# Performance work log

Measured on AMD Instinct MI355X. Metric: run time of the kernel, lower is better.

## Reference

```python
import jax, jax.numpy as jnp
import numpy as np

B, TX, TY = 32, 64, 64
E = H = 1024
VEN = VCN = 32000


def _lstm_scan(x_gates, Whh, bhh, h0, c0):
    # x_gates: [T, B, 4H] precomputed input contribution (x @ Wih.T + bih)
    def step(carry, xg_t):
        h, c = carry
        gates = xg_t + h @ Whh.T + bhh  # [B, 4H]
        i, f, g, o = jnp.split(gates, 4, axis=-1)  # torch gate order i,f,g,o
        c = jax.nn.sigmoid(f) * c + jax.nn.sigmoid(i) * jnp.tanh(g)
        h = jax.nn.sigmoid(o) * jnp.tanh(c)
        return (h, c), (h, c)
    (hT, cT), (hs, cs) = jax.lax.scan(step, (h0, c0), x_gates)
    return hs, cs, hT, cT  # hs/cs: [T, B, H]


def setup_inputs() -> dict:
    key = jax.random.key(0)
    ks = jax.random.split(key, 12)
    u = lambda k, shp, s: jax.random.uniform(k, shp, jnp.float32, -s, s)
    s = 1.0 / np.sqrt(H)
    return {
        "x": jax.random.randint(ks[0], (B, TX), 0, VEN, dtype=jnp.int32),
        "x_mask": jnp.ones((B, TX), dtype=jnp.int32),
        "y": jax.random.randint(ks[1], (B, TY), 0, VCN, dtype=jnp.int32),
        "h0": jnp.zeros((B, H), jnp.float32),
        "c0": jnp.zeros((B, H), jnp.float32),
        "emb_en": u(ks[2], (VEN, E), 0.1),
        "emb_cn": u(ks[3], (VCN, E), 0.1),
        "Wih_e": u(ks[4], (4 * H, E), s),
        "Whh_e": u(ks[5], (4 * H, H), s),
        "bih_e": jnp.zeros((4 * H,), jnp.float32),
        "bhh_e": jnp.zeros((4 * H,), jnp.float32),
        "Wih_d": u(ks[6], (4 * H, E), s),
        "Whh_d": u(ks[7], (4 * H, H), s),
        "bih_d": jnp.zeros((4 * H,), jnp.float32),
        "bhh_d": jnp.zeros((4 * H,), jnp.float32),
        "Wout": u(ks[8], (VCN, H), 0.1),
        "bout": jnp.zeros((VCN,), jnp.float32),
    }


def reference(x, x_mask, y, h0, c0, emb_en, emb_cn,
              Wih_e, Whh_e, bih_e, bhh_e,
              Wih_d, Whh_d, bih_d, bhh_d, Wout, bout):
    # --- encoder: per-timestep LSTMCell unrolled via lax.scan ---
    xe = emb_en[x]  # [B, Tx, E]
    xg = jnp.einsum('bte,ge->tbg', xe, Wih_e) + bih_e  # [Tx, B, 4H]
    hs, cs, _, _ = _lstm_scan(xg, Whh_e, bhh_e, h0, c0)  # [Tx, B, H]
    # pick hidden/cell at last valid timestep (mask.sum - 1)
    lengths = jnp.sum(x_mask, axis=1) - 1  # [B]
    bidx = jnp.arange(x.shape[0])
    h = hs[lengths, bidx]  # [B, H]
    c = cs[lengths, bidx]
    # --- decoder: single-layer LSTM ---
    ye = emb_cn[y]  # [B, Ty, E]
    yg = jnp.einsum('bte,ge->tbg', ye, Wih_d) + bih_d  # [Ty, B, 4H]
    dh, _, _, _ = _lstm_scan(yg, Whh_d, bhh_d, h, c)  # [Ty, B, H]
    hiddens = jnp.transpose(dh, (1, 0, 2))  # [B, Ty, H]
    logits = jnp.einsum('bth,vh->btv', hiddens, Wout) + bout  # [B, Ty, V]
    decoded = jax.nn.log_softmax(logits, axis=-1)
    return decoded, hiddens
```

## Files before the change

kernel.cpp:

```cpp
#include <hip/hip_runtime.h>

typedef __attribute__((ext_vector_type(8))) short bf16x8;
typedef __attribute__((ext_vector_type(4))) float fx4;
typedef __attribute__((ext_vector_type(4))) unsigned short u16x4;
typedef __attribute__((ext_vector_type(8))) unsigned short u16x8;
typedef __attribute__((ext_vector_type(4))) unsigned int u32x4;

#define DEV static __device__ __forceinline__

DEV unsigned short f2bf(float f) {
  union { float f; unsigned u; } v; v.f = f;
  unsigned u = v.u;
  u += 0x7fffu + ((u >> 16) & 1u);
  return (unsigned short)(u >> 16);
}
DEV unsigned pk(float a, float b) { return (unsigned)f2bf(a) | ((unsigned)f2bf(b) << 16); }
DEV float sigm(float x) { return 1.f / (1.f + __expf(-x)); }

DEV u32x4 load_coh16(const void* p) {
  u32x4 r;
  asm volatile("global_load_dwordx4 %0, %1, off sc0 sc1" : "=v"(r) : "v"(p));
  return r;
}

typedef __attribute__((address_space(1))) const unsigned int guint;
typedef __attribute__((address_space(3))) unsigned int luint;
DEV void gload_lds16(const void* g, void* l) {
  __builtin_amdgcn_global_load_lds((guint*)g, (luint*)l, 16, 0, 0);
}

__global__ void k_gather2(const float* __restrict__ embE, const int* __restrict__ tokE,
                          unsigned short* __restrict__ dstE,
                          const float* __restrict__ embC, const int* __restrict__ tokC,
                          unsigned short* __restrict__ dstC) {
  int bid = blockIdx.x;
  int r = bid & 2047;
  const float* emb = bid < 2048 ? embE : embC;
  const int* tok = bid < 2048 ? tokE : tokC;
  unsigned short* dst = bid < 2048 ? dstE : dstC;
  int t = r >> 5, b = r & 31;
  int token = tok[b * 64 + t];
  const fx4* srow = (const fx4*)(emb + (long)token * 1024);
  u16x4* drow = (u16x4*)(dst + (long)r * 1024);
  fx4 v = srow[threadIdx.x];
  u16x4 o = { f2bf(v[0]), f2bf(v[1]), f2bf(v[2]), f2bf(v[3]) };
  drow[threadIdx.x] = o;
}

__global__ void k_lengths(const int* __restrict__ mask, int* __restrict__ sel,
                          int* __restrict__ bar) {
  int t = threadIdx.x;
  for (int i = t; i < 4096; i += 256) bar[i] = 0;
  if (t < 32) {
    int s = 0;
    for (int k = 0; k < 64; ++k) s += mask[t * 64 + k];
    sel[t] = (s + 63) & 63;
  }
}

__global__ void k_f2bf_dual(const float* __restrict__ s0, unsigned short* __restrict__ d0,
                            const float* __restrict__ s1, unsigned short* __restrict__ d1,
                            long n4) {
  const float* s = blockIdx.x < 1024 ? s0 : s1;
  unsigned short* d = blockIdx.x < 1024 ? d0 : d1;
  long base = (long)(blockIdx.x & 1023) * 256 + threadIdx.x;
  for (long i = base; i < n4; i += 1024 * 256) {
    fx4 v = ((const fx4*)s)[i];
    u16x4 o = { f2bf(v[0]), f2bf(v[1]), f2bf(v[2]), f2bf(v[3]) };
    ((u16x4*)d)[i] = o;
  }
}

#define SCAN_NBLK 64

template<int MODE>
__global__ __launch_bounds__(512) void k_scan(
    const float* __restrict__ Whh,
    const float* __restrict__ bhh,
    const float* __restrict__ xg,
    const float* __restrict__ hinit,
    const float* __restrict__ cinit,
    unsigned short* __restrict__ hbuf,
    const int* __restrict__ sel,
    float* __restrict__ hsel, float* __restrict__ csel,
    float* __restrict__ hid_out,
    unsigned short* __restrict__ hid_bf,
    int* __restrict__ bar,
    const float* __restrict__ wsrc,
    unsigned short* __restrict__ wdst,
    long wn4) {
  int tid = threadIdx.x;
  int bid = blockIdx.x;
  if (bid >= SCAN_NBLK) {
    long i = (long)(bid - SCAN_NBLK) * 512 + tid;
    long st = (long)(gridDim.x - SCAN_NBLK) * 512;
    for (; i < wn4; i += st) {
      fx4 v = ((const fx4*)wsrc)[i];
      u16x4 o = { f2bf(v[0]), f2bf(v[1]), f2bf(v[2]), f2bf(v[3]) };
      ((u16x4*)wdst)[i] = o;
    }
    return;
  }
  __shared__ __align__(16) unsigned short hlds[49152];
  __shared__ float gbuf[4][32][16];
  int j0 = ((bid & 7) * 8 + (bid >> 3)) * 16;
  int w = tid >> 6, lane = tid & 63;
  int mt = w & 1, nt = w >> 1;
  int fr = lane & 15, fg = lane >> 4;
  unsigned* hbU = (unsigned*)hbuf;
  constexpr int GBASE = MODE ? 64 : 0;

  bf16x8 breg[32];
  {
    const float* wrow = Whh + ((long)(nt * 1024 + j0 + fr) << 10);
#pragma unroll
    for (int i = 0; i < 32; ++i) {
      int kc = i * 4 + fg;
      fx4 lo = *(const fx4*)(wrow + kc * 8);
      fx4 hi = *(const fx4*)(wrow + kc * 8 + 4);
      bf16x8 o = { (short)f2bf(lo[0]), (short)f2bf(lo[1]), (short)f2bf(lo[2]), (short)f2bf(lo[3]),
                   (short)f2bf(hi[0]), (short)f2bf(hi[1]), (short)f2bf(hi[2]), (short)f2bf(hi[3]) };
      breg[i] = o;
    }
  }

  int b = tid >> 4, jj = tid & 15, j = j0 + jj;
  float bh0 = bhh[j], bh1 = bhh[1024 + j], bh2 = bhh[2048 + j], bh3 = bhh[3072 + j];
  float c_reg = cinit[b * 1024 + j];
  int sel_b = (MODE == 0) ? sel[b] : -1;
  const float* xp0 = xg + (long)b * 4096 + j;
  float x0 = xp0[0], x1 = xp0[1024], x2 = xp0[2048], x3 = xp0[3072];

  for (int t = 0; t < 64; ++t) {
    if (t == 0) {
#pragma unroll
      for (int it = 0; it < 8; ++it) {
        int c = it * 512 + tid;
        const float* src = hinit + (long)c * 8;
        fx4 lo = *(const fx4*)src;
        fx4 hi = *(const fx4*)(src + 4);
        int row = c >> 7, kc = c & 127;
        u16x8 o = { f2bf(lo[0]), f2bf(lo[1]), f2bf(lo[2]), f2bf(lo[3]),
                    f2bf(hi[0]), f2bf(hi[1]), f2bf(hi[2]), f2bf(hi[3]) };
        *(u16x8*)&hlds[(row * 128 + (kc ^ (row & 31))) * 8] = o;
      }
    } else {
      const char* hsrc = (const char*)hbuf + (t & 1) * 65536;
      u32x4 hv[8];
#pragma unroll
      for (int it = 0; it < 8; ++it) {
        int c = it * 512 + tid;
        hv[it] = load_coh16(hsrc + (long)c * 16);
      }
      asm volatile("s_waitcnt vmcnt(0)" ::: "memory");
      __builtin_amdgcn_sched_barrier(0);
#pragma unroll
      for (int it = 0; it < 8; ++it) {
        int c = it * 512 + tid;
        int row = c >> 7, kc = c & 127;
        *(u16x8*)&hlds[(row * 128 + (kc ^ (row & 31))) * 8] = *(u16x8*)&hv[it];
      }
    }
    __syncthreads();

    int arow = mt * 16 + fr;
    fx4 acca = {0.f, 0.f, 0.f, 0.f}, accb = {0.f, 0.f, 0.f, 0.f};
#pragma unroll
    for (int i = 0; i < 32; i += 2) {
      int kcA = i * 4 + fg;
      int kcB = (i + 1) * 4 + fg;
      bf16x8 a0 = *(const bf16x8*)&hlds[(arow * 128 + (kcA ^ (arow & 31))) * 8];
      bf16x8 a1 = *(const bf16x8*)&hlds[(arow * 128 + (kcB ^ (arow & 31))) * 8];
      acca = __builtin_amdgcn_mfma_f32_16x16x32_bf16(a0, breg[i], acca, 0, 0, 0);
      accb = __builtin_amdgcn_mfma_f32_16x16x32_bf16(a1, breg[i + 1], accb, 0, 0, 0);
    }
#pragma unroll
    for (int q = 0; q < 4; ++q)
      gbuf[nt][mt * 16 + fg * 4 + q][fr] = acca[q] + accb[q];
    __syncthreads();

    {
      float gi = gbuf[0][b][jj] + bh0 + x0;
      float gf = gbuf[1][b][jj] + bh1 + x1;
      float gg = gbuf[2][b][jj] + bh2 + x2;
      float go = gbuf[3][b][jj] + bh3 + x3;
      float c_new = sigm(gf) * c_reg + sigm(gi) * tanhf(gg);
      float h = sigm(go) * tanhf(c_new);
      c_reg = c_new;
      float hp = __shfl_xor(h, 1);
      if ((jj & 1) == 0) {
        unsigned val = pk(h, hp);
        __hip_atomic_store(&hbU[((t & 1) ^ 1) * 16384 + b * 512 + ((j0 + jj) >> 1)], val,
                           __ATOMIC_RELAXED, __HIP_MEMORY_SCOPE_AGENT);
      }
      if (MODE == 0) {
        if (t == sel_b) { hsel[b * 1024 + j] = h; csel[b * 1024 + j] = c_new; }
      } else {
        long o = ((long)b * 64 + t) * 1024 + j;
        hid_out[o] = h;
        if (hid_bf) hid_bf[o] = f2bf(h);
      }
    }

    if (t < 63) {
      const float* xp = xg + (long)(t + 1) * 131072 + (long)b * 4096 + j;
      float nx0 = xp[0], nx1 = xp[1024], nx2 = xp[2048], nx3 = xp[3072];
      __syncthreads();
      if (w == 0) {
        if (lane == 0)
          __hip_atomic_store(&bar[bid * 32], GBASE + t + 1, __ATOMIC_RELAXED, __HIP_MEMORY_SCOPE_AGENT);
        int want = GBASE + t + 1;
        for (;;) {
          int v0 = __hip_atomic_load(&bar[lane * 32], __ATOMIC_RELAXED, __HIP_MEMORY_SCOPE_AGENT);
          if (__ballot(v0 >= want) == 0xFFFFFFFFFFFFFFFFULL) break;
          __builtin_amdgcn_s_sleep(1);
        }
      }
      __syncthreads();
      x0 = nx0; x1 = nx1; x2 = nx2; x3 = nx3;
    }
  }
}

__global__ __launch_bounds__(256) void k_gemm_dual(
    const unsigned short* __restrict__ A0, const unsigned short* __restrict__ B0,
    const float* __restrict__ bias0, float* __restrict__ C0,
    const unsigned short* __restrict__ A1, const unsigned short* __restrict__ B1,
    const float* __restrict__ bias1, float* __restrict__ C1) {
  __shared__ __align__(16) unsigned short As[2][4096];
  __shared__ __align__(16) unsigned short Bs[2][4096];
  int lid = blockIdx.x;
  int half = lid >> 9, l = lid & 511;
  const unsigned short* A = half ? A1 : A0;
  const unsigned short* Bw = half ? B1 : B0;
  const float* bias = half ? bias1 : bias0;
  float* C = half ? C1 : C0;
  int swz = (l & 7) * 64 + (l >> 3);
  long m0 = (long)(swz & 15) * 128;
  long n0 = (long)(swz >> 4) * 128;
  int tid = threadIdx.x, lane = tid & 63, w = tid >> 6;
  int mw = (w & 1) * 64, nw = (w >> 1) * 64;
  int fr = lane & 15, fg = lane >> 4;
  fx4 acc[4][4] = {};
  int c0 = tid, c1 = tid + 256;
  int r0 = c0 >> 2, k0s = (c0 & 3) ^ ((r0 >> 1) & 3);
  int r1 = c1 >> 2, k1s = (c1 & 3) ^ ((r1 >> 1) & 3);
  const unsigned short* gA0 = A + (m0 + r0) * 1024 + k0s * 8;
  const unsigned short* gA1 = A + (m0 + r1) * 1024 + k1s * 8;
  const unsigned short* gB0 = Bw + (n0 + r0) * 1024 + k0s * 8;
  const unsigned short* gB1 = Bw + (n0 + r1) * 1024 + k1s * 8;
  auto stage = [&](int buf, int kt) {
    int k0 = kt * 32;
    gload_lds16(gA0 + k0, &As[buf][c0 * 8]);
    gload_lds16(gA1 + k0, &As[buf][c1 * 8]);
    gload_lds16(gB0 + k0, &Bs[buf][c0 * 8]);
    gload_lds16(gB1 + k0, &Bs[buf][c1 * 8]);
  };
  stage(0, 0);
  __syncthreads();
  for (int kt = 0; kt < 32; ++kt) {
    int cur = kt & 1;
    if (kt < 31) stage(cur ^ 1, kt + 1);
    bf16x8 af[4], bfr[4];
#pragma unroll
    for (int mi = 0; mi < 4; ++mi) {
      int row = mw + mi * 16 + fr;
      af[mi] = *(const bf16x8*)&As[cur][(row * 4 + (fg ^ ((row >> 1) & 3))) * 8];
    }
#pragma unroll
    for (int ni = 0; ni < 4; ++ni) {
      int row = nw + ni * 16 + fr;
      bfr[ni] = *(const bf16x8*)&Bs[cur][(row * 4 + (fg ^ ((row >> 1) & 3))) * 8];
    }
#pragma unroll
    for (int mi = 0; mi < 4; ++mi)
#pragma unroll
      for (int ni = 0; ni < 4; ++ni)
        acc[mi][ni] = __builtin_amdgcn_mfma_f32_16x16x32_bf16(af[mi], bfr[ni], acc[mi][ni], 0, 0, 0);
    __syncthreads();
  }
#pragma unroll
  for (int ni = 0; ni < 4; ++ni) {
    long n = n0 + nw + ni * 16 + fr;
    float bs = bias[n];
#pragma unroll
    for (int mi = 0; mi < 4; ++mi) {
      long rbase = m0 + mw + mi * 16 + fg * 4;
#pragma unroll
      for (int q = 0; q < 4; ++q)
        C[(rbase + q) * 4096 + n] = acc[mi][ni][q] + bs;
    }
  }
}

__global__ __launch_bounds__(256) void k_gemm_bb(const unsigned short* __restrict__ A,
                                                 const unsigned short* __restrict__ Bw,
                                                 const float* __restrict__ bias,
                                                 float* __restrict__ C) {
  __shared__ __align__(16) unsigned short As[2][4096];
  __shared__ __align__(16) unsigned short Bs[2][4096];
  int lid = blockIdx.x;
  int swz = (lid & 7) * 500 + (lid >> 3);
  long m0 = (long)(swz & 15) * 128;
  long n0 = (long)(swz >> 4) * 128;
  int tid = threadIdx.x, lane = tid & 63, w = tid >> 6;
  int mw = (w & 1) * 64, nw = (w >> 1) * 64;
  int fr = lane & 15, fg = lane >> 4;
  fx4 acc[4][4] = {};
  int c0 = tid, c1 = tid + 256;
  int r0 = c0 >> 2, k0s = (c0 & 3) ^ ((r0 >> 1) & 3);
  int r1 = c1 >> 2, k1s = (c1 & 3) ^ ((r1 >> 1) & 3);
  const unsigned short* gA0 = A + (m0 + r0) * 1024 + k0s * 8;
  const unsigned short* gA1 = A + (m0 + r1) * 1024 + k1s * 8;
  const unsigned short* gB0 = Bw + (n0 + r0) * 1024 + k0s * 8;
  const unsigned short* gB1 = Bw + (n0 + r1) * 1024 + k1s * 8;
  auto stage = [&](int buf, int kt) {
    int k0 = kt * 32;
    gload_lds16(gA0 + k0, &As[buf][c0 * 8]);
    gload_lds16(gA1 + k0, &As[buf][c1 * 8]);
    gload_lds16(gB0 + k0, &Bs[buf][c0 * 8]);
    gload_lds16(gB1 + k0, &Bs[buf][c1 * 8]);
  };
  stage(0, 0);
  __syncthreads();
  for (int kt = 0; kt < 32; ++kt) {
    int cur = kt & 1;
    if (kt < 31) stage(cur ^ 1, kt + 1);
    bf16x8 af[4], bfr[4];
#pragma unroll
    for (int mi = 0; mi < 4; ++mi) {
      int row = mw + mi * 16 + fr;
      af[mi] = *(const bf16x8*)&As[cur][(row * 4 + (fg ^ ((row >> 1) & 3))) * 8];
    }
#pragma unroll
    for (int ni = 0; ni < 4; ++ni) {
      int row = nw + ni * 16 + fr;
      bfr[ni] = *(const bf16x8*)&Bs[cur][(row * 4 + (fg ^ ((row >> 1) & 3))) * 8];
    }
#pragma unroll
    for (int mi = 0; mi < 4; ++mi)
#pragma unroll
      for (int ni = 0; ni < 4; ++ni)
        acc[mi][ni] = __builtin_amdgcn_mfma_f32_16x16x32_bf16(bfr[ni], af[mi], acc[mi][ni], 0, 0, 0);
    __syncthreads();
  }
#pragma unroll
  for (int mi = 0; mi < 4; ++mi) {
    long m = m0 + mw + mi * 16 + fr;
#pragma unroll
    for (int ni = 0; ni < 4; ++ni) {
      long nbase = n0 + nw + ni * 16 + fg * 4;
      fx4 bs4 = *(const fx4*)&bias[nbase];
      fx4 o = { acc[mi][ni][0] + bs4[0], acc[mi][ni][1] + bs4[1],
                acc[mi][ni][2] + bs4[2], acc[mi][ni][3] + bs4[3] };
      *(fx4*)&C[m * 32000 + nbase] = o;
    }
  }
}

template<typename TA, typename TB>
__global__ __launch_bounds__(256) void k_gemm(const TA* __restrict__ A,
                                              const TB* __restrict__ Bw,
                                              const float* __restrict__ bias,
                                              float* __restrict__ C,
                                              int ldc, int q8) {
  __shared__ __align__(16) unsigned short As[2][4096];
  __shared__ __align__(16) unsigned short Bs[2][4096];
  int lid = blockIdx.x;
  int swz = (lid & 7) * q8 + (lid >> 3);
  long m0 = (long)(swz & 15) * 128;
  long n0 = (long)(swz >> 4) * 128;
  int tid = threadIdx.x, lane = tid & 63, w = tid >> 6;
  int mw = (w & 1) * 64, nw = (w >> 1) * 64;
  int fr = lane & 15, fg = lane >> 4;
  fx4 acc[4][4] = {};

  int crow[2], kc[2], phys[2];
#pragma unroll
  for (int u = 0; u < 2; ++u) {
    int c = tid + u * 256;
    crow[u] = c >> 2; kc[u] = c & 3;
    phys[u] = crow[u] * 4 + (kc[u] ^ ((crow[u] >> 1) & 3));
  }
  u32x4 ra[2], rb[2];
  auto loadOne = [&](const auto* P, long row, int u) -> u32x4 {
    long off = row * 1024 + kc[u] * 8;
    if constexpr (sizeof(*P) == 2) {
      return *(const u32x4*)(P + off);
    } else {
      fx4 lo = *(const fx4*)(P + off);
      fx4 hi = *(const fx4*)(P + off + 4);
      u32x4 r = { pk(lo[0], lo[1]), pk(lo[2], lo[3]), pk(hi[0], hi[1]), pk(hi[2], hi[3]) };
      return r;
    }
  };
  auto loadRegs = [&](int kt) {
#pragma unroll
    for (int u = 0; u < 2; ++u) {
      ra[u] = loadOne(A + (long)kt * 32, m0 + crow[u], u);
      rb[u] = loadOne(Bw + (long)kt * 32, n0 + crow[u], u);
    }
  };
  auto storeRegs = [&](int buf) {
#pragma unroll
    for (int u = 0; u < 2; ++u) {
      *(u32x4*)&As[buf][phys[u] * 8] = ra[u];
      *(u32x4*)&Bs[buf][phys[u] * 8] = rb[u];
    }
  };
  loadRegs(0);
  storeRegs(0);
  __syncthreads();
  for (int kt = 0; kt < 32; ++kt) {
    int cur = kt & 1;
    if (kt < 31) loadRegs(kt + 1);
    bf16x8 af[4], bf_[4];
#pragma unroll
    for (int mi = 0; mi < 4; ++mi) {
      int row = mw + mi * 16 + fr;
      af[mi] = *(const bf16x8*)&As[cur][(row * 4 + (fg ^ ((row >> 1) & 3))) * 8];
    }
#pragma unroll
    for (int ni = 0; ni < 4; ++ni) {
      int row = nw + ni * 16 + fr;
      bf_[ni] = *(const bf16x8*)&Bs[cur][(row * 4 + (fg ^ ((row >> 1) & 3))) * 8];
    }
#pragma unroll
    for (int mi = 0; mi < 4; ++mi)
#pragma unroll
      for (int ni = 0; ni < 4; ++ni)
        acc[mi][ni] = __builtin_amdgcn_mfma_f32_16x16x32_bf16(af[mi], bf_[ni], acc[mi][ni], 0, 0, 0);
    if (kt < 31) storeRegs((kt + 1) & 1);
    __syncthreads();
  }
#pragma unroll
  for (int ni = 0; ni < 4; ++ni) {
    long n = n0 + nw + ni * 16 + fr;
    float bs = bias[n];
#pragma unroll
    for (int mi = 0; mi < 4; ++mi) {
      long rbase = m0 + mw + mi * 16 + fg * 4;
#pragma unroll
      for (int q = 0; q < 4; ++q)
        C[(rbase + q) * ldc + n] = acc[mi][ni][q] + bs;
    }
  }
}

__global__ __launch_bounds__(256) void k_logsoftmax(float* __restrict__ logits) {
  long base = (long)blockIdx.x * 32000;
  float* row = logits + base;
  int tid = threadIdx.x;
  __shared__ float redm[4], reds[4];
  float m = -3.4e38f, s = 0.f;
  for (int i = tid; i < 8000; i += 256) {
    fx4 v = ((const fx4*)row)[i];
    float cm = fmaxf(fmaxf(v[0], v[1]), fmaxf(v[2], v[3]));
    if (cm > m) { s *= __expf(m - cm); m = cm; }
    s += __expf(v[0] - m) + __expf(v[1] - m) + __expf(v[2] - m) + __expf(v[3] - m);
  }
  for (int o = 32; o; o >>= 1) {
    float m2 = __shfl_xor(m, o), s2 = __shfl_xor(s, o);
    float mn = fmaxf(m, m2);
    s = s * __expf(m - mn) + s2 * __expf(m2 - mn);
    m = mn;
  }
  if ((tid & 63) == 0) { redm[tid >> 6] = m; reds[tid >> 6] = s; }
  __syncthreads();
  float M = fmaxf(fmaxf(redm[0], redm[1]), fmaxf(redm[2], redm[3]));
  float S = reds[0] * __expf(redm[0] - M) + reds[1] * __expf(redm[1] - M) +
            reds[2] * __expf(redm[2] - M) + reds[3] * __expf(redm[3] - M);
  float lse = M + logf(S);
  for (int i = tid; i < 8000; i += 256) {
    fx4 v = ((const fx4*)row)[i];
    fx4 o = { v[0] - lse, v[1] - lse, v[2] - lse, v[3] - lse };
    ((fx4*)row)[i] = o;
  }
}

extern "C" void kernel_launch(void* const* d_in, const int* in_sizes, int n_in,
                              void* d_out, int out_size, void* d_ws, size_t ws_size,
                              hipStream_t stream) {
  const int*   x     = (const int*)d_in[0];
  const int*   xmask = (const int*)d_in[1];
  const int*   y     = (const int*)d_in[2];
  const float* h0    = (const float*)d_in[3];
  const float* c0    = (const float*)d_in[4];
  const float* embE  = (const float*)d_in[5];
  const float* embC  = (const float*)d_in[6];
  const float* WihE  = (const float*)d_in[7];
  const float* WhhE  = (const float*)d_in[8];
  const float* bihE  = (const float*)d_in[9];
  const float* bhhE  = (const float*)d_in[10];
  const float* WihD  = (const float*)d_in[11];
  const float* WhhD  = (const float*)d_in[12];
  const float* bihD  = (const float*)d_in[13];
  const float* bhhD  = (const float*)d_in[14];
  const float* Wout  = (const float*)d_in[15];
  const float* bout  = (const float*)d_in[16];

  float* out = (float*)d_out;
  float* decoded = out;
  float* hiddens = out + 65536000L;

  float* xg_e = decoded;
  float* xg_d = decoded + 8388608L;
  unsigned short* xe_bf   = (unsigned short*)(decoded + 16777216L);
  unsigned short* ye_bf   = xe_bf + 2097152L;
  unsigned short* WihE_bf = ye_bf + 2097152L;
  unsigned short* WihD_bf = WihE_bf + 4194304L;
  char* sp = (char*)(WihD_bf + 4194304L);
  unsigned short* hbuf = (unsigned short*)sp; sp += 2 * 32768 * 2;
  float* hsel = (float*)sp; sp += 32768 * 4;
  float* csel = (float*)sp; sp += 32768 * 4;
  int* sel = (int*)sp; sp += 256;
  int* bar = (int*)sp; sp += 16384;

  unsigned short* hid_bf  = (unsigned short*)d_ws;
  unsigned short* Wout_bf = hid_bf + 2097152L;
  size_t need1 = 2048L * 1024 * 2;
  size_t need2 = need1 + 32000L * 1024 * 2;
  bool fast1 = ws_size >= need1;
  bool fast2 = ws_size >= need2;

  k_gather2<<<4096, 256, 0, stream>>>(embE, x, xe_bf, embC, y, ye_bf);
  k_lengths<<<1, 256, 0, stream>>>(xmask, sel, bar);
  k_f2bf_dual<<<2048, 256, 0, stream>>>(WihE, WihE_bf, WihD, WihD_bf, 1048576L);

  k_gemm_dual<<<1024, 256, 0, stream>>>(xe_bf, WihE_bf, bihE, xg_e,
                                        ye_bf, WihD_bf, bihD, xg_d);

  k_scan<0><<<SCAN_NBLK + (fast2 ? 192 : 0), 512, 0, stream>>>(
      WhhE, bhhE, xg_e, h0, c0, hbuf, sel, hsel, csel, nullptr, nullptr, bar,
      Wout, Wout_bf, fast2 ? 8192000L : 0L);
  k_scan<1><<<SCAN_NBLK, 512, 0, stream>>>(
      WhhD, bhhD, xg_d, hsel, csel, hbuf, nullptr, nullptr, nullptr, hiddens,
      fast1 ? hid_bf : nullptr, bar, nullptr, nullptr, 0L);

  if (fast2)      k_gemm_bb<<<4000, 256, 0, stream>>>(hid_bf, Wout_bf, bout, decoded);
  else if (fast1) k_gemm<unsigned short, float><<<4000, 256, 0, stream>>>(hid_bf, Wout, bout, decoded, 32000, 500);
  else            k_gemm<float, float><<<4000, 256, 0, stream>>>(hiddens, Wout, bout, decoded, 32000, 500);
  k_logsoftmax<<<2048, 256, 0, stream>>>(decoded);
}
```

Measured before the change: 901.5 us.

## Fuse encoder and decoder LSTM scans into one persistent kernel

Merges the two scan launches into a single persistent kernel. It runs the encoder steps, keeps the selected h/c in registers, reloads the decoder weights and continues with the decoder steps, using one grid barrier between phases. This removes a kernel launch and the global hsel/csel round trip. It also changes the k_gemm_bb tile mapping so the 250 N-tiles lie along the fast index, which changes L2 reuse of the output projection. The cost is register pressure and a serial reload of Whh inside the persistent blocks.

```diff
diff --git a/kernel.cpp b/kernel.cpp
--- a/kernel.cpp
+++ b/kernel.cpp
@@ -73,16 +73,14 @@
 
 #define SCAN_NBLK 64
 
-template<int MODE>
-__global__ __launch_bounds__(512) void k_scan(
-    const float* __restrict__ Whh,
-    const float* __restrict__ bhh,
-    const float* __restrict__ xg,
-    const float* __restrict__ hinit,
-    const float* __restrict__ cinit,
+__global__ __launch_bounds__(512) void k_scan_all(
+    const float* __restrict__ WhhE, const float* __restrict__ bhhE,
+    const float* __restrict__ xg_e,
+    const float* __restrict__ WhhD, const float* __restrict__ bhhD,
+    const float* __restrict__ xg_d,
+    const float* __restrict__ h0, const float* __restrict__ c0,
     unsigned short* __restrict__ hbuf,
     const int* __restrict__ sel,
-    float* __restrict__ hsel, float* __restrict__ csel,
     float* __restrict__ hid_out,
     unsigned short* __restrict__ hid_bf,
     int* __restrict__ bar,
@@ -108,10 +106,22 @@
   int mt = w & 1, nt = w >> 1;
   int fr = lane & 15, fg = lane >> 4;
   unsigned* hbU = (unsigned*)hbuf;
-  constexpr int GBASE = MODE ? 64 : 0;
-
-  bf16x8 breg[32];
-  {
+
+  auto gridbar = [&](int gen) {
+    __syncthreads();
+    if (w == 0) {
+      if (lane == 0)
+        __hip_atomic_store(&bar[bid * 32], gen, __ATOMIC_RELAXED, __HIP_MEMORY_SCOPE_AGENT);
+      for (;;) {
+        int v0 = __hip_atomic_load(&bar[lane * 32], __ATOMIC_RELAXED, __HIP_MEMORY_SCOPE_AGENT);
+        if (__ballot(v0 >= gen) == 0xFFFFFFFFFFFFFFFFULL) break;
+        __builtin_amdgcn_s_sleep(1);
+      }
+    }
+    __syncthreads();
+  };
+
+  auto loadBreg = [&](const float* Whh, bf16x8* breg) {
     const float* wrow = Whh + ((long)(nt * 1024 + j0 + fr) << 10);
 #pragma unroll
     for (int i = 0; i < 32; ++i) {
@@ -122,13 +132,17 @@
                    (short)f2bf(hi[0]), (short)f2bf(hi[1]), (short)f2bf(hi[2]), (short)f2bf(hi[3]) };
       breg[i] = o;
     }
-  }
+  };
+
+  bf16x8 breg[32];
+  loadBreg(WhhE, breg);
 
   int b = tid >> 4, jj = tid & 15, j = j0 + jj;
-  float bh0 = bhh[j], bh1 = bhh[1024 + j], bh2 = bhh[2048 + j], bh3 = bhh[3072 + j];
-  float c_reg = cinit[b * 1024 + j];
-  int sel_b = (MODE == 0) ? sel[b] : -1;
-  const float* xp0 = xg + (long)b * 4096 + j;
+  float bh0 = bhhE[j], bh1 = bhhE[1024 + j], bh2 = bhhE[2048 + j], bh3 = bhhE[3072 + j];
+  float c_reg = c0[b * 1024 + j];
+  int sel_b = sel[b];
+  float hsel_reg = 0.f, csel_reg = 0.f;
+  const float* xp0 = xg_e + (long)b * 4096 + j;
   float x0 = xp0[0], x1 = xp0[1024], x2 = xp0[2048], x3 = xp0[3072];
 
   for (int t = 0; t < 64; ++t) {
@@ -136,7 +150,7 @@
 #pragma unroll
       for (int it = 0; it < 8; ++it) {
         int c = it * 512 + tid;
-        const float* src = hinit + (long)c * 8;
+        const float* src = h0 + (long)c * 8;
         fx4 lo = *(const fx4*)src;
         fx4 hi = *(const fx4*)(src + 4);
         int row = c >> 7, kc = c & 127;
@@ -167,8 +181,7 @@
     fx4 acca = {0.f, 0.f, 0.f, 0.f}, accb = {0.f, 0.f, 0.f, 0.f};
 #pragma unroll
     for (int i = 0; i < 32; i += 2) {
-      int kcA = i * 4 + fg;
-      int kcB = (i + 1) * 4 + fg;
+      int kcA = i * 4 + fg, kcB = (i + 1) * 4 + fg;
       bf16x8 a0 = *(const bf16x8*)&hlds[(arow * 128 + (kcA ^ (arow & 31))) * 8];
       bf16x8 a1 = *(const bf16x8*)&hlds[(arow * 128 + (kcB ^ (arow & 31))) * 8];
       acca = __builtin_amdgcn_mfma_f32_16x16x32_bf16(a0, breg[i], acca, 0, 0, 0);
@@ -189,34 +202,90 @@
       c_reg = c_new;
       float hp = __shfl_xor(h, 1);
       if ((jj & 1) == 0) {
-        unsigned val = pk(h, hp);
-        __hip_atomic_store(&hbU[((t & 1) ^ 1) * 16384 + b * 512 + ((j0 + jj) >> 1)], val,
-                           __ATOMIC_RELAXED, __HIP_MEMORY_SCOPE_AGENT);
+        __hip_atomic_store(&hbU[((t & 1) ^ 1) * 16384 + b * 512 + ((j0 + jj) >> 1)],
+                           pk(h, hp), __ATOMIC_RELAXED, __HIP_MEMORY_SCOPE_AGENT);
       }
-      if (MODE == 0) {
-        if (t == sel_b) { hsel[b * 1024 + j] = h; csel[b * 1024 + j] = c_new; }
-      } else {
-        long o = ((long)b * 64 + t) * 1024 + j;
-        hid_out[o] = h;
-        if (hid_bf) hid_bf[o] = f2bf(h);
+      if (t == sel_b) { hsel_reg = h; csel_reg = c_new; }
+    }
+
+    if (t < 63) {
+      const float* xp = xg_e + (long)(t + 1) * 131072 + (long)b * 4096 + j;
+      float nx0 = xp[0], nx1 = xp[1024], nx2 = xp[2048], nx3 = xp[3072];
+      gridbar(t + 1);
+      x0 = nx0; x1 = nx1; x2 = nx2; x3 = nx3;
+    }
+  }
+
+  loadBreg(WhhD, breg);
+  bh0 = bhhD[j]; bh1 = bhhD[1024 + j]; bh2 = bhhD[2048 + j]; bh3 = bhhD[3072 + j];
+  c_reg = csel_reg;
+  {
+    float hp = __shfl_xor(hsel_reg, 1);
+    if ((jj & 1) == 0)
+      __hip_atomic_store(&hbU[b * 512 + ((j0 + jj) >> 1)],
+                         pk(hsel_reg, hp), __ATOMIC_RELAXED, __HIP_MEMORY_SCOPE_AGENT);
+  }
+  {
+    const float* xp = xg_d + (long)b * 4096 + j;
+    x0 = xp[0]; x1 = xp[1024]; x2 = xp[2048]; x3 = xp[3072];
+  }
+  gridbar(64);
+
+  for (int t2 = 0; t2 < 64; ++t2) {
+    const char* hsrc = (const char*)hbuf + (t2 & 1) * 65536;
+    u32x4 hv[8];
+#pragma unroll
+    for (int it = 0; it < 8; ++it) {
+      int c = it * 512 + tid;
+      hv[it] = load_coh16(hsrc + (long)c * 16);
+    }
+    asm volatile("s_waitcnt vmcnt(0)" ::: "memory");
+    __builtin_amdgcn_sched_barrier(0);
+#pragma unroll
+    for (int it = 0; it < 8; ++it) {
+      int c = it * 512 + tid;
+      int row = c >> 7, kc = c & 127;
+      *(u16x8*)&hlds[(row * 128 + (kc ^ (row & 31))) * 8] = *(u16x8*)&hv[it];
+    }
+    __syncthreads();
+
+    int arow = mt * 16 + fr;
+    fx4 acca = {0.f, 0.f, 0.f, 0.f}, accb = {0.f, 0.f, 0.f, 0.f};
+#pragma unroll
+    for (int i = 0; i < 32; i += 2) {
+      int kcA = i * 4 + fg, kcB = (i + 1) * 4 + fg;
+      bf16x8 a0 = *(const bf16x8*)&hlds[(arow * 128 + (kcA ^ (arow & 31))) * 8];
+      bf16x8 a1 = *(const bf16x8*)&hlds[(arow * 128 + (kcB ^ (arow & 31))) * 8];
+      acca = __builtin_amdgcn_mfma_f32_16x16x32_bf16(a0, breg[i], acca, 0, 0, 0);
+      accb = __builtin_amdgcn_mfma_f32_16x16x32_bf16(a1, breg[i + 1], accb, 0, 0, 0);
+    }
+#pragma unroll
+    for (int q = 0; q < 4; ++q)
+      gbuf[nt][mt * 16 + fg * 4 + q][fr] = acca[q] + accb[q];
+    __syncthreads();
+
+    {
+      float gi = gbuf[0][b][jj] + bh0 + x0;
+      float gf = gbuf[1][b][jj] + bh1 + x1;
+      float gg = gbuf[2][b][jj] + bh2 + x2;
+      float go = gbuf[3][b][jj] + bh3 + x3;
+      float c_new = sigm(gf) * c_reg + sigm(gi) * tanhf(gg);
+      float h = sigm(go) * tanhf(c_new);
+      c_reg = c_new;
+      float hp = __shfl_xor(h, 1);
+      if ((jj & 1) == 0) {
+        __hip_atomic_store(&hbU[((t2 & 1) ^ 1) * 16384 + b * 512 + ((j0 + jj) >> 1)],
+                           pk(h, hp), __ATOMIC_RELAXED, __HIP_MEMORY_SCOPE_AGENT);
       }
-    }
-
-    if (t < 63) {
-      const float* xp = xg + (long)(t + 1) * 131072 + (long)b * 4096 + j;
+      long o = ((long)b * 64 + t2) * 1024 + j;
+      hid_out[o] = h;
+      if (hid_bf) hid_bf[o] = f2bf(h);
+    }
+
+    if (t2 < 63) {
+      const float* xp = xg_d + (long)(t2 + 1) * 131072 + (long)b * 4096 + j;
       float nx0 = xp[0], nx1 = xp[1024], nx2 = xp[2048], nx3 = xp[3072];
-      __syncthreads();
-      if (w == 0) {
-        if (lane == 0)
-          __hip_atomic_store(&bar[bid * 32], GBASE + t + 1, __ATOMIC_RELAXED, __HIP_MEMORY_SCOPE_AGENT);
-        int want = GBASE + t + 1;
-        for (;;) {
-          int v0 = __hip_atomic_load(&bar[lane * 32], __ATOMIC_RELAXED, __HIP_MEMORY_SCOPE_AGENT);
-          if (__ballot(v0 >= want) == 0xFFFFFFFFFFFFFFFFULL) break;
-          __builtin_amdgcn_s_sleep(1);
-        }
-      }
-      __syncthreads();
+      gridbar(65 + t2);
       x0 = nx0; x1 = nx1; x2 = nx2; x3 = nx3;
     }
   }
@@ -301,8 +370,8 @@
   __shared__ __align__(16) unsigned short Bs[2][4096];
   int lid = blockIdx.x;
   int swz = (lid & 7) * 500 + (lid >> 3);
-  long m0 = (long)(swz & 15) * 128;
-  long n0 = (long)(swz >> 4) * 128;
+  long m0 = (long)(swz / 250) * 128;
+  long n0 = (long)(swz % 250) * 128;
   int tid = threadIdx.x, lane = tid & 63, w = tid >> 6;
   int mw = (w & 1) * 64, nw = (w >> 1) * 64;
   int fr = lane & 15, fg = lane >> 4;
@@ -511,8 +580,6 @@
   unsigned short* WihD_bf = WihE_bf + 4194304L;
   char* sp = (char*)(WihD_bf + 4194304L);
   unsigned short* hbuf = (unsigned short*)sp; sp += 2 * 32768 * 2;
-  float* hsel = (float*)sp; sp += 32768 * 4;
-  float* csel = (float*)sp; sp += 32768 * 4;
   int* sel = (int*)sp; sp += 256;
   int* bar = (int*)sp; sp += 16384;
 
@@ -523,19 +590,16 @@
   bool fast1 = ws_size >= need1;
   bool fast2 = ws_size >= need2;
 
+  k_lengths<<<1, 256, 0, stream>>>(xmask, sel, bar);
   k_gather2<<<4096, 256, 0, stream>>>(embE, x, xe_bf, embC, y, ye_bf);
-  k_lengths<<<1, 256, 0, stream>>>(xmask, sel, bar);
   k_f2bf_dual<<<2048, 256, 0, stream>>>(WihE, WihE_bf, WihD, WihD_bf, 1048576L);
 
   k_gemm_dual<<<1024, 256, 0, stream>>>(xe_bf, WihE_bf, bihE, xg_e,
                                         ye_bf, WihD_bf, bihD, xg_d);
 
-  k_scan<0><<<SCAN_NBLK + (fast2 ? 192 : 0), 512, 0, stream>>>(
-      WhhE, bhhE, xg_e, h0, c0, hbuf, sel, hsel, csel, nullptr, nullptr, bar,
-      Wout, Wout_bf, fast2 ? 8192000L : 0L);
-  k_scan<1><<<SCAN_NBLK, 512, 0, stream>>>(
-      WhhD, bhhD, xg_d, hsel, csel, hbuf, nullptr, nullptr, nullptr, hiddens,
-      fast1 ? hid_bf : nullptr, bar, nullptr, nullptr, 0L);
+  k_scan_all<<<SCAN_NBLK + (fast2 ? 192 : 0), 512, 0, stream>>>(
+      WhhE, bhhE, xg_e, WhhD, bhhD, xg_d, h0, c0, hbuf, sel, hiddens,
+      fast1 ? hid_bf : nullptr, bar, Wout, Wout_bf, fast2 ? 8192000L : 0L);
 
   if (fast2)      k_gemm_bb<<<4000, 256, 0, stream>>>(hid_bf, Wout_bf, bout, decoded);
   else if (fast1) k_gemm<unsigned short, float><<<4000, 256, 0, stream>>>(hid_bf, Wout, bout, decoded, 32000, 500);
```

Result: slower. 922.4 us (+2.3%).
